# Performance work log

Hardware: AMD Instinct MI355X
Metric: run time of the kernel (lower is better)

Reference implementation:

```python
import jax, jax.numpy as jnp
import numpy as np

EMBED_DIM = 1024
B, S = 4, 2048
SCALE = float(np.sqrt(EMBED_DIM))


def setup_inputs() -> dict:
    key = jax.random.key(0)
    ks = jax.random.split(key, 9)
    d = EMBED_DIM
    init = 1.0 / np.sqrt(d)
    return {
        "query": jax.random.normal(ks[0], (B, S, d), jnp.float32),
        "key": jax.random.normal(ks[1], (B, S, d), jnp.float32),
        "value": jax.random.normal(ks[2], (B, S, d), jnp.float32),
        "wq": jax.random.uniform(ks[3], (d, d), jnp.float32, -init, init),
        "bq": jax.random.uniform(ks[4], (d,), jnp.float32, -init, init),
        "wk": jax.random.uniform(ks[5], (d, d), jnp.float32, -init, init),
        "bk": jax.random.uniform(ks[6], (d,), jnp.float32, -init, init),
        "wv": jax.random.uniform(ks[7], (d, d), jnp.float32, -init, init),
        "bv": jax.random.uniform(ks[8], (d,), jnp.float32, -init, init),
    }


def reference(query, key, value, wq, bq, wk, bk, wv, bv):
    # Linear projections (torch Linear: x @ W^T + b; here weights stored as [in, out])
    q = query @ wq + bq            # [B,S,D]
    k = key @ wk + bk              # [B,S,D]
    v = value @ wv + bv            # [B,S,D]
    scores = jnp.einsum("bqd,bkd->bqk", q, k) / SCALE   # [B,S,S]
    attn = jax.nn.softmax(scores, axis=-1)
    # dropout in eval mode -> identity
    return jnp.einsum("bqk,bkd->bqd", attn, v)          # [B,S,D]
```

## Files before the change

kernel.cpp:

```cpp
#include <hip/hip_runtime.h>
#include <hip/hip_bf16.h>

typedef __attribute__((ext_vector_type(4))) float   f32x4;
typedef __attribute__((ext_vector_type(8))) __bf16  bf16x8;
typedef __attribute__((ext_vector_type(4))) __bf16  bf16x4;

#define NB 4
#define SS 2048
#define DD 1024

__device__ __forceinline__ void gload_lds16(const void* g, void* l) {
  __builtin_amdgcn_global_load_lds((const __attribute__((address_space(1))) void*)g,
                                   (__attribute__((address_space(3))) void*)l,
                                   16, 0, 0);
}

__global__ __launch_bounds__(256) void prep_w_kernel(
    const float* __restrict__ wq, const float* __restrict__ wk, const float* __restrict__ wv,
    const float* __restrict__ bq, const float* __restrict__ bk, const float* __restrict__ bv,
    __bf16* __restrict__ Wt, float* __restrict__ biasbuf)
{
  const int z = blockIdx.z;
  const float* W  = z == 0 ? wq : (z == 1 ? wk : wv);
  const float* bi = z == 0 ? bq : (z == 1 ? bk : bv);
  __bf16* dst = Wt + (size_t)z * (size_t)(DD * DD);
  const int n0 = blockIdx.x * 32, k0 = blockIdx.y * 32;
  __shared__ float t[32][33];
  const int tx = threadIdx.x & 31, ty = threadIdx.x >> 5;
  #pragma unroll
  for (int i = 0; i < 4; i++)
    t[ty + 8 * i][tx] = W[(size_t)(k0 + ty + 8 * i) * DD + n0 + tx];
  __syncthreads();
  #pragma unroll
  for (int i = 0; i < 4; i++)
    dst[(size_t)(n0 + ty + 8 * i) * DD + k0 + tx] = (__bf16)t[tx][ty + 8 * i];
  if (blockIdx.x == 0 && blockIdx.y == 0) {
    #pragma unroll
    for (int i = 0; i < 4; i++)
      biasbuf[z * DD + threadIdx.x + 256 * i] = bi[threadIdx.x + 256 * i];
  }
}


#define PJ_A_OFF(BUF)     ((BUF) * 16384)
#define PJ_B_OFF(BUF, NH) (32768 + ((BUF)*2 + (NH)) * 16384)

#define PJ_DSA(BUF)                                                             \
  _Pragma("unroll") for (int mi = 0; mi < 4; ++mi) {                            \
    _Pragma("unroll") for (int ks = 0; ks < 2; ++ks)                            \
      af[mi][ks] = *(const bf16x8*)(smem + PJ_A_OFF(BUF) + ara[ks] + mi * 2048); }

#define PJ_DSB(DST, BUF, NH)                                                    \
  _Pragma("unroll") for (int ni = 0; ni < 2; ++ni) {                            \
    _Pragma("unroll") for (int ks = 0; ks < 2; ++ks)                            \
      DST[ni][ks] = *(const bf16x8*)(smem + PJ_B_OFF(BUF, NH) + brb2[ks] + ni * 2048); }

#define PJ_GLA(V0, V1, V2, V3, T) do { int t_ = (T); if (t_ >= 16) t_ = 0;      \
  const float* g_ = Ablk + (size_t)t_ * 64;                                     \
  V0 = *(const float4*)(g_ + aoffF0); V1 = *(const float4*)(g_ + aoffF0 + 4);   \
  V2 = *(const float4*)(g_ + aoffF1); V3 = *(const float4*)(g_ + aoffF1 + 4);   \
  __builtin_amdgcn_sched_barrier(0); } while (0)

#define PJ_WRA(BUF, V0, V1, V2, V3) do {                                        \
  bf16x8 w0_, w1_;                                                              \
  w0_[0]=(__bf16)V0.x; w0_[1]=(__bf16)V0.y; w0_[2]=(__bf16)V0.z; w0_[3]=(__bf16)V0.w; \
  w0_[4]=(__bf16)V1.x; w0_[5]=(__bf16)V1.y; w0_[6]=(__bf16)V1.z; w0_[7]=(__bf16)V1.w; \
  w1_[0]=(__bf16)V2.x; w1_[1]=(__bf16)V2.y; w1_[2]=(__bf16)V2.z; w1_[3]=(__bf16)V2.w; \
  w1_[4]=(__bf16)V3.x; w1_[5]=(__bf16)V3.y; w1_[6]=(__bf16)V3.z; w1_[7]=(__bf16)V3.w; \
  *(bf16x8*)(smem + PJ_A_OFF(BUF) + tid * 16) = w0_;                            \
  *(bf16x8*)(smem + PJ_A_OFF(BUF) + 8192 + tid * 16) = w1_; } while (0)

#define PJ_SB0(BUF, T) do { int t_ = (T); if (t_ >= 16) t_ = 0;                 \
  const __bf16* gB_ = Bblk + (size_t)t_ * 64;                                   \
  gload_lds16(gB_ + boff0, smem + PJ_B_OFF(BUF, 0) + tid * 16);                 \
  gload_lds16(gB_ + boff1, smem + PJ_B_OFF(BUF, 0) + 8192 + tid * 16); } while (0)

#define PJ_SB1(BUF, T) do { int t_ = (T); if (t_ >= 16) t_ = 0;                 \
  const __bf16* gB_ = Bblk + (size_t)(128 * 1024) + (size_t)t_ * 64;            \
  gload_lds16(gB_ + boff0, smem + PJ_B_OFF(BUF, 1) + tid * 16);                 \
  gload_lds16(gB_ + boff1, smem + PJ_B_OFF(BUF, 1) + 8192 + tid * 16); } while (0)

#define PJ_MFMA(BF, NH) do {                                                    \
  __builtin_amdgcn_s_barrier();                                                 \
  asm volatile("s_waitcnt lgkmcnt(0)" ::: "memory");                            \
  __builtin_amdgcn_sched_barrier(0);                                            \
  __builtin_amdgcn_s_setprio(1);                                                \
  _Pragma("unroll") for (int mi = 0; mi < 4; ++mi)                              \
  _Pragma("unroll") for (int ni = 0; ni < 2; ++ni)                              \
  _Pragma("unroll") for (int ks = 0; ks < 2; ++ks)                              \
    acc[mi][(NH)*2+ni] = __builtin_amdgcn_mfma_f32_16x16x32_bf16(               \
        af[mi][ks], BF[ni][ks], acc[mi][(NH)*2+ni], 0, 0, 0);                   \
  __builtin_amdgcn_s_setprio(0);                                                \
  __builtin_amdgcn_sched_barrier(0);                                            \
  __builtin_amdgcn_s_barrier(); } while (0)

__global__ __launch_bounds__(512) void proj_kernel(
    const float* __restrict__ Xq, const float* __restrict__ Xk, const float* __restrict__ Xv,
    const __bf16* __restrict__ Wt, const float* __restrict__ bias,
    __bf16* __restrict__ Qo, __bf16* __restrict__ Ko, __bf16* __restrict__ Vt)
{
  extern __shared__ char smem[];

  const int gx = gridDim.x, gy = gridDim.y;
  const int nwg = gx * gy * gridDim.z;
  int lin = blockIdx.x + gx * (blockIdx.y + gy * blockIdx.z);
  const int cpx = nwg >> 3;
  int swz = (lin & 7) * cpx + (lin >> 3);
  const int bx = swz % gx;
  int rem = swz / gx;
  const int by = rem % gy;
  const int bz = rem / gy;

  const long brow = (long)by * 128, bcol = (long)bx * 256;
  const float* Xsel = bz == 0 ? Xq : (bz == 1 ? Xk : Xv);
  const float* Ablk = Xsel + (size_t)brow * 1024;
  const __bf16* Bblk = Wt + (size_t)bz * (DD * DD) + (size_t)bcol * 1024;

  const int tid  = threadIdx.x;
  const int lane = tid & 63;
  const int wid  = tid >> 6;
  const int wm = wid >> 2, wn = wid & 3;
  const int l15 = lane & 15, l4 = lane >> 4;
  const int lx = (lane & 7) << 4;

  int aoffF0, aoffF1;
  #pragma unroll
  for (int i = 0; i < 2; ++i) {
    const int p = i * 8192 + tid * 16;
    const int r = p >> 7;
    const int kb = (p ^ ((r & 7) << 4)) & 127;
    const int aF = r * 1024 + (kb >> 1);
    if (i == 0) aoffF0 = aF; else aoffF1 = aF;
  }
  int boff0, boff1;
  #pragma unroll
  for (int i = 0; i < 2; ++i) {
    const int p = i * 8192 + tid * 16;
    const int r = p >> 7;
    const int kb = (p ^ ((r & 7) << 4)) & 127;
    const int off = r * 1024 + (kb >> 1);
    if (i == 0) boff0 = off; else boff1 = off;
  }

  int ara[2], brb2[2];
  #pragma unroll
  for (int ks = 0; ks < 2; ++ks) {
    ara[ks]  = ((((wm * 64 + l15) * 64 + l4 * 8) * 2) + ks * 64) ^ lx;
    brb2[ks] = ((((wn * 32 + l15) * 64 + l4 * 8) * 2) + ks * 64) ^ lx;
  }

  f32x4 acc[4][4] = {};
  bf16x8 af[4][2], b0[2][2], b1[2][2];
  float4 La0, La1, La2, La3, Lb0, Lb1, Lb2, Lb3;

  PJ_GLA(La0, La1, La2, La3, 0);
  PJ_GLA(Lb0, Lb1, Lb2, Lb3, 1);
  PJ_SB0(0, 0); PJ_SB1(0, 0); PJ_SB0(1, 1);
  asm volatile("s_waitcnt vmcnt(10)" ::: "memory");
  PJ_WRA(0, La0, La1, La2, La3);
  asm volatile("s_waitcnt vmcnt(6)" ::: "memory");
  PJ_WRA(1, Lb0, Lb1, Lb2, Lb3);
  asm volatile("s_waitcnt vmcnt(2) lgkmcnt(0)" ::: "memory");
  __builtin_amdgcn_s_barrier();

  for (int it = 0; it < 8; ++it) {
    const int tt = it * 2;
    PJ_GLA(La0, La1, La2, La3, tt + 2);
    PJ_SB1(1, tt + 1);
    PJ_DSA(0); PJ_DSB(b0, 0, 0);
    PJ_MFMA(b0, 0);
    PJ_SB0(0, tt + 2);
    asm volatile("s_waitcnt vmcnt(10)" ::: "memory");
    PJ_DSB(b1, 0, 1);
    PJ_MFMA(b1, 1);
    asm volatile("s_waitcnt vmcnt(4)" ::: "memory");
    PJ_WRA(0, La0, La1, La2, La3);
    PJ_GLA(Lb0, Lb1, Lb2, Lb3, tt + 3);
    PJ_SB1(0, tt + 2);
    PJ_DSA(1); PJ_DSB(b0, 1, 0);
    PJ_MFMA(b0, 0);
    PJ_SB0(1, tt + 3);
    asm volatile("s_waitcnt vmcnt(4)" ::: "memory");
    PJ_WRA(1, Lb0, Lb1, Lb2, Lb3);
    PJ_DSB(b1, 1, 1);
    PJ_MFMA(b1, 1);
  }

  if (bz == 2) {
    #pragma unroll
    for (int mi = 0; mi < 4; ++mi) {
      #pragma unroll
      for (int n = 0; n < 4; ++n) {
        const long row = brow + wm * 64 + mi * 16 + l4 * 4;
        const long col = bcol + (n >> 1) * 128 + wn * 32 + (n & 1) * 16 + l15;
        const float bvv = bias[2 * DD + col];
        const long bb = row >> 11, s = row & 2047;
        bf16x4 pk = { (__bf16)(acc[mi][n][0] + bvv), (__bf16)(acc[mi][n][1] + bvv),
                      (__bf16)(acc[mi][n][2] + bvv), (__bf16)(acc[mi][n][3] + bvv) };
        *(bf16x4*)&Vt[bb * 2097152 + col * 2048 + s] = pk;
      }
    }
  } else {
    __bf16* C = bz == 0 ? Qo : Ko;
    #pragma unroll
    for (int mi = 0; mi < 4; ++mi) {
      #pragma unroll
      for (int n = 0; n < 4; ++n) {
        const long row = brow + wm * 64 + mi * 16 + l4 * 4;
        const long col = bcol + (n >> 1) * 128 + wn * 32 + (n & 1) * 16 + l15;
        const float bvv = bias[bz * DD + col];
        #pragma unroll
        for (int e = 0; e < 4; ++e)
          C[(row + e) * 1024 + col] = (__bf16)(acc[mi][n][e] + bvv);
      }
    }
  }
}


#define A_OFF(BUF, MH) (((BUF)*2 + (MH)) * 16384)
#define B_OFF(BUF, NH) (65536 + ((BUF)*2 + (NH)) * 16384)

#define STAGE_A(BUF, MH, T) do { int t_ = (T); if (t_ >= NT) t_ = 0;            \
  const __bf16* gs_ = Ablk + (size_t)(MH) * (64 * (size_t)lda) + (size_t)t_ * 64; \
  gload_lds16(gs_ + aoff0, smem + A_OFF(BUF, MH) + tid * 16);                    \
  gload_lds16(gs_ + aoff1, smem + A_OFF(BUF, MH) + 8192 + tid * 16); } while (0)

#define STAGE_B(BUF, NH, T) do { int t_ = (T); if (t_ >= NT) t_ = 0;            \
  const __bf16* gs_ = Bblk + (size_t)(NH) * (32 * (size_t)ldb) + (size_t)t_ * 64; \
  gload_lds16(gs_ + boff0, smem + B_OFF(BUF, NH) + tid * 16);                    \
  gload_lds16(gs_ + boff1, smem + B_OFF(BUF, NH) + 8192 + tid * 16); } while (0)

#define DSREAD_A(DST, BUF, MH)                                                  \
  _Pragma("unroll") for (int mi = 0; mi < 4; ++mi) {                            \
    _Pragma("unroll") for (int ks = 0; ks < 2; ++ks)                            \
      DST[mi][ks] = *(const bf16x8*)(smem + A_OFF(BUF, MH) + arb[ks] + mi * 2048); }

#define DSREAD_BS(DST, BUF, NH)                                                 \
  _Pragma("unroll") for (int ni = 0; ni < 2; ++ni) {                            \
    _Pragma("unroll") for (int ks = 0; ks < 2; ++ks)                            \
      DST[ni][ks] = *(const bf16x8*)(smem + B_OFF(BUF, NH) + brb[ks] + ni * 2048); }

#define BARRIER_MFMA(AF, BF, MH, NH) do {                                       \
  __builtin_amdgcn_s_barrier();                                                 \
  asm volatile("s_waitcnt lgkmcnt(0)" ::: "memory");                            \
  __builtin_amdgcn_sched_barrier(0);                                            \
  __builtin_amdgcn_s_setprio(1);                                                \
  _Pragma("unroll") for (int mi = 0; mi < 4; ++mi)                              \
  _Pragma("unroll") for (int ni = 0; ni < 2; ++ni)                              \
  _Pragma("unroll") for (int ks = 0; ks < 2; ++ks)                              \
    acc[(MH)*4+mi][(NH)*2+ni] = __builtin_amdgcn_mfma_f32_16x16x32_bf16(        \
        AF[mi][ks], BF[ni][ks], acc[(MH)*4+mi][(NH)*2+ni], 0, 0, 0);            \
  __builtin_amdgcn_s_setprio(0);                                                \
  __builtin_amdgcn_sched_barrier(0);                                            \
  __builtin_amdgcn_s_barrier(); } while (0)

__global__ __launch_bounds__(512) void gemm8p_kernel(
    const __bf16* __restrict__ A, const __bf16* __restrict__ B,
    float scale, void* __restrict__ Cout,
    int K, int lda, int ldb, int ldc,
    long strideA, long strideB, long strideC)
{
  extern __shared__ char smem[];

  const int gx = gridDim.x, gy = gridDim.y;
  const int nwg = gx * gy * gridDim.z;
  int lin = blockIdx.x + gx * (blockIdx.y + gy * blockIdx.z);
  const int cpx = nwg >> 3;
  int swz = (lin & 7) * cpx + (lin >> 3);
  const int bx = swz % gx;
  int rem = swz / gx;
  const int by = rem % gy;
  const int bz = rem / gy;

  const long brow = (long)by * 256, bcol = (long)bx * 256;
  const __bf16* Ablk = A + (size_t)bz * strideA + (size_t)brow * lda;
  const __bf16* Bblk = B + (size_t)bz * strideB + (size_t)bcol * ldb;

  const int tid  = threadIdx.x;
  const int lane = tid & 63;
  const int wid  = tid >> 6;
  const int wm = wid >> 2, wn = wid & 3;
  const int l15 = lane & 15, l4 = lane >> 4;
  const int lx = (lane & 7) << 4;

  const int NT = K >> 6;
  const int niter = NT >> 1;

  int aoff0, aoff1, boff0, boff1;
  #pragma unroll
  for (int i = 0; i < 2; ++i) {
    const int p = i * 8192 + tid * 16;
    const int l = p ^ (((p >> 7) & 7) << 4);
    const int r = p >> 7;
    const int kb = l & 127;
    const int av = ((r >> 6) * 128 + (r & 63)) * lda + (kb >> 1);
    const int bv = ((r >> 5) * 64 + (r & 31)) * ldb + (kb >> 1);
    if (i == 0) { aoff0 = av; boff0 = bv; } else { aoff1 = av; boff1 = bv; }
  }

  int arb[2], brb[2];
  #pragma unroll
  for (int ks = 0; ks < 2; ++ks) {
    arb[ks] = ((((wm * 64 + l15) * 64 + l4 * 8) * 2) + ks * 64) ^ lx;
    brb[ks] = ((((wn * 32 + l15) * 64 + l4 * 8) * 2) + ks * 64) ^ lx;
  }

  f32x4 acc[8][4] = {};
  bf16x8 a0[4][2], a1[4][2], b0[2][2], b1[2][2];

  STAGE_B(0, 0, 0); STAGE_A(0, 0, 0); STAGE_A(0, 1, 0); STAGE_B(0, 1, 0);
  STAGE_B(1, 0, 1); STAGE_A(1, 0, 1);
  asm volatile("s_waitcnt vmcnt(4)" ::: "memory");
  __builtin_amdgcn_s_barrier();

  for (int it = 0; it < niter; ++it) {
    const int tt = it * 2;
    DSREAD_A(a0, 0, 0); DSREAD_BS(b0, 0, 0);
    STAGE_A(1, 1, tt + 1);
    BARRIER_MFMA(a0, b0, 0, 0);
    DSREAD_A(a1, 0, 1);
    STAGE_B(1, 1, tt + 1);
    BARRIER_MFMA(a1, b0, 1, 0);
    DSREAD_BS(b1, 0, 1);
    STAGE_B(0, 0, tt + 2);
    BARRIER_MFMA(a0, b1, 0, 1);
    STAGE_A(0, 0, tt + 2);
    asm volatile("s_waitcnt vmcnt(4)" ::: "memory");
    BARRIER_MFMA(a1, b1, 1, 1);
    DSREAD_A(a0, 1, 0); DSREAD_BS(b0, 1, 0);
    STAGE_A(0, 1, tt + 2);
    BARRIER_MFMA(a0, b0, 0, 0);
    DSREAD_A(a1, 1, 1);
    STAGE_B(0, 1, tt + 2);
    BARRIER_MFMA(a1, b0, 1, 0);
    DSREAD_BS(b1, 1, 1);
    STAGE_B(1, 0, tt + 3);
    BARRIER_MFMA(a0, b1, 0, 1);
    STAGE_A(1, 0, tt + 3);
    asm volatile("s_waitcnt vmcnt(4)" ::: "memory");
    BARRIER_MFMA(a1, b1, 1, 1);
  }

  const int cr = l4 * 4;
  __bf16* C = (__bf16*)Cout + (size_t)bz * strideC;
  #pragma unroll
  for (int m = 0; m < 8; ++m) {
    #pragma unroll
    for (int n = 0; n < 4; ++n) {
      const long row = brow + wm * 128 + m * 16 + cr;
      const long col = bcol + wn * 64 + n * 16 + l15;
      #pragma unroll
      for (int e = 0; e < 4; ++e)
        C[(row + e) * (size_t)ldc + col] = (__bf16)__expf(acc[m][n][e] * scale);
    }
  }
}


#define PV_A_OFF(BUF)     ((BUF) * 16384)
#define PV_B_OFF(BUF, NH) (32768 + ((BUF)*2 + (NH)) * 16384)

#define PV_DSA(BUF)                                                             \
  _Pragma("unroll") for (int mi = 0; mi < 4; ++mi) {                            \
    _Pragma("unroll") for (int ks = 0; ks < 2; ++ks)                            \
      af[mi][ks] = *(const bf16x8*)(smem + PV_A_OFF(BUF) + ara[ks] + mi * 2048); }

#define PV_DSB(DST, BUF, NH)                                                    \
  _Pragma("unroll") for (int ni = 0; ni < 2; ++ni) {                            \
    _Pragma("unroll") for (int ks = 0; ks < 2; ++ks)                            \
      DST[ni][ks] = *(const bf16x8*)(smem + PV_B_OFF(BUF, NH) + brb2[ks] + ni * 2048); }

#define PV_SA(BUF, T) do { int t_ = (T); if (t_ >= NT) t_ = 0;                  \
  const __bf16* gA_ = Ablk + (size_t)t_ * 64;                                   \
  gload_lds16(gA_ + aoff0, smem + PV_A_OFF(BUF) + tid * 16);                    \
  gload_lds16(gA_ + aoff1, smem + PV_A_OFF(BUF) + 8192 + tid * 16);             \
  const __bf16* gB_ = Bblk + (size_t)t_ * 64;                                   \
  gload_lds16(gB_ + boff0, smem + PV_B_OFF(BUF, 0) + tid * 16);                 \
  gload_lds16(gB_ + boff1, smem + PV_B_OFF(BUF, 0) + 8192 + tid * 16); } while (0)

#define PV_SB(BUF, T) do { int t_ = (T); if (t_ >= NT) t_ = 0;                  \
  const __bf16* gB_ = Bblk + (size_t)(128 * (size_t)ldb) + (size_t)t_ * 64;     \
  gload_lds16(gB_ + boff0, smem + PV_B_OFF(BUF, 1) + tid * 16);                 \
  gload_lds16(gB_ + boff1, smem + PV_B_OFF(BUF, 1) + 8192 + tid * 16); } while (0)

#define PV_MFMA(BF, NH, DOSUM) do {                                             \
  __builtin_amdgcn_s_barrier();                                                 \
  asm volatile("s_waitcnt lgkmcnt(0)" ::: "memory");                            \
  __builtin_amdgcn_sched_barrier(0);                                            \
  __builtin_amdgcn_s_setprio(1);                                                \
  _Pragma("unroll") for (int mi = 0; mi < 4; ++mi)                              \
  _Pragma("unroll") for (int ni = 0; ni < 2; ++ni)                              \
  _Pragma("unroll") for (int ks = 0; ks < 2; ++ks)                              \
    acc[mi][(NH)*2+ni] = __builtin_amdgcn_mfma_f32_16x16x32_bf16(               \
        af[mi][ks], BF[ni][ks], acc[mi][(NH)*2+ni], 0, 0, 0);                   \
  if (DOSUM) {                                                                  \
    _Pragma("unroll") for (int mi = 0; mi < 4; ++mi)                            \
    _Pragma("unroll") for (int ks = 0; ks < 2; ++ks)                            \
      accs[mi] = __builtin_amdgcn_mfma_f32_16x16x32_bf16(                       \
          af[mi][ks], onesf, accs[mi], 0, 0, 0); }                              \
  __builtin_amdgcn_s_setprio(0);                                                \
  __builtin_amdgcn_sched_barrier(0);                                            \
  __builtin_amdgcn_s_barrier(); } while (0)

__global__ __launch_bounds__(512) void gemm128_kernel(
    const __bf16* __restrict__ A, const __bf16* __restrict__ B,
    void* __restrict__ Cout,
    int K, int lda, int ldb, int ldc,
    long strideA, long strideB, long strideC)
{
  extern __shared__ char smem[];

  const int gx = gridDim.x, gy = gridDim.y;
  const int nwg = gx * gy * gridDim.z;
  int lin = blockIdx.x + gx * (blockIdx.y + gy * blockIdx.z);
  const int cpx = nwg >> 3;
  int swz = (lin & 7) * cpx + (lin >> 3);
  const int bx = swz % gx;
  int rem = swz / gx;
  const int by = rem % gy;
  const int bz = rem / gy;

  const long brow = (long)by * 128, bcol = (long)bx * 256;
  const __bf16* Ablk = A + (size_t)bz * strideA + (size_t)brow * lda;
  const __bf16* Bblk = B + (size_t)bz * strideB + (size_t)bcol * ldb;

  const int tid  = threadIdx.x;
  const int lane = tid & 63;
  const int wid  = tid >> 6;
  const int wm = wid >> 2, wn = wid & 3;
  const int l15 = lane & 15, l4 = lane >> 4;
  const int lx = (lane & 7) << 4;

  const int NT = K >> 6;
  const int niter = NT >> 1;

  int aoff0, aoff1, boff0, boff1;
  #pragma unroll
  for (int i = 0; i < 2; ++i) {
    const int p = i * 8192 + tid * 16;
    const int r = p >> 7;
    const int kb = (p ^ ((r & 7) << 4)) & 127;
    const int av = r * lda + (kb >> 1);
    const int bv = r * ldb + (kb >> 1);
    if (i == 0) { aoff0 = av; boff0 = bv; } else { aoff1 = av; boff1 = bv; }
  }

  int ara[2], brb2[2];
  #pragma unroll
  for (int ks = 0; ks < 2; ++ks) {
    ara[ks]  = ((((wm * 64 + l15) * 64 + l4 * 8) * 2) + ks * 64) ^ lx;
    brb2[ks] = ((((wn * 32 + l15) * 64 + l4 * 8) * 2) + ks * 64) ^ lx;
  }

  f32x4 acc[4][4] = {};
  f32x4 accs[4] = {};
  bf16x8 af[4][2], b0[2][2], b1[2][2];
  bf16x8 onesf;
  #pragma unroll
  for (int j = 0; j < 8; ++j) onesf[j] = (__bf16)1.0f;

  PV_SA(0, 0); PV_SB(0, 0); PV_SA(1, 1);
  asm volatile("s_waitcnt vmcnt(6)" ::: "memory");
  __builtin_amdgcn_s_barrier();

  for (int it = 0; it < niter; ++it) {
    const int tt = it * 2;
    PV_SB(1, tt + 1);
    asm volatile("s_waitcnt vmcnt(6)" ::: "memory");
    PV_DSA(0); PV_DSB(b0, 0, 0);
    PV_MFMA(b0, 0, 1);
    PV_SA(0, tt + 2);
    asm volatile("s_waitcnt vmcnt(6)" ::: "memory");
    PV_DSB(b1, 0, 1);
    PV_MFMA(b1, 1, 0);
    PV_SB(0, tt + 2);
    asm volatile("s_waitcnt vmcnt(6)" ::: "memory");
    PV_DSA(1); PV_DSB(b0, 1, 0);
    PV_MFMA(b0, 0, 1);
    PV_SA(1, tt + 3);
    asm volatile("s_waitcnt vmcnt(6)" ::: "memory");
    PV_DSB(b1, 1, 1);
    PV_MFMA(b1, 1, 0);
  }

  float* C = (float*)Cout + (size_t)bz * strideC;
  #pragma unroll
  for (int mi = 0; mi < 4; ++mi) {
    f32x4 inv;
    #pragma unroll
    for (int e = 0; e < 4; ++e) inv[e] = 1.0f / accs[mi][e];
    #pragma unroll
    for (int n = 0; n < 4; ++n) {
      const long row = brow + wm * 64 + mi * 16 + l4 * 4;
      const long col = bcol + (n >> 1) * 128 + wn * 32 + (n & 1) * 16 + l15;
      #pragma unroll
      for (int e = 0; e < 4; ++e)
        C[(row + e) * (size_t)ldc + col] = acc[mi][n][e] * inv[e];
    }
  }
}

extern "C" void kernel_launch(void* const* d_in, const int* in_sizes, int n_in,
                              void* d_out, int out_size, void* d_ws, size_t ws_size,
                              hipStream_t stream)
{
  const float* query = (const float*)d_in[0];
  const float* key   = (const float*)d_in[1];
  const float* value = (const float*)d_in[2];
  const float* wq = (const float*)d_in[3];
  const float* bq = (const float*)d_in[4];
  const float* wk = (const float*)d_in[5];
  const float* bk = (const float*)d_in[6];
  const float* wv = (const float*)d_in[7];
  const float* bv = (const float*)d_in[8];

  char* ws = (char*)d_ws;
  __bf16* P       = (__bf16*)(ws + 0);
  __bf16* Wt      = (__bf16*)(ws + 33554432);
  float*  biasbuf = (float*)(ws + 39845888);
  __bf16* Qb      = (__bf16*)(ws + 39858176);
  __bf16* Kb      = (__bf16*)(ws + 56635392);
  __bf16* Vt      = (__bf16*)(ws + 73412608);

  hipFuncSetAttribute((const void*)proj_kernel,    hipFuncAttributeMaxDynamicSharedMemorySize, 131072);
  hipFuncSetAttribute((const void*)gemm8p_kernel,  hipFuncAttributeMaxDynamicSharedMemorySize, 131072);
  hipFuncSetAttribute((const void*)gemm128_kernel, hipFuncAttributeMaxDynamicSharedMemorySize, 131072);

  dim3 b256(256), b512(512);

  prep_w_kernel<<<dim3(32, 32, 3), b256, 0, stream>>>(wq, wk, wv, bq, bk, bv, Wt, biasbuf);

  proj_kernel<<<dim3(4, 64, 3), b512, 98304, stream>>>(
      query, key, value, Wt, biasbuf, Qb, Kb, Vt);

  gemm8p_kernel<<<dim3(8, 8, 4), b512, 131072, stream>>>(
      Qb, Kb, 0.03125f, P,
      1024, 1024, 1024, 2048,
      2097152L, 2097152L, 4194304L);

  gemm128_kernel<<<dim3(4, 16, 4), b512, 98304, stream>>>(
      P, Vt, d_out,
      2048, 2048, 2048, 1024,
      4194304L, 2097152L, 2097152L);

  (void)in_sizes; (void)n_in; (void)out_size; (void)ws_size;
}
```

Measured before the change: 169.1 us.

## Pre-convert fp32 activations to bf16 and stream projection A tiles via direct LDS loads

Adds a separate kernel that converts query, key and value from fp32 to bf16 into workspace. The projection GEMM then loads both A and B tiles with global-to-LDS async loads, dropping the register staging and in-loop fp32-to-bf16 conversion along with its VGPR pressure. The cost is an extra pass over 100MB of fp32 input plus writing 50MB of bf16, which may outweigh the simpler pipeline since the projection re-reads each A tile only a few times.

```diff
diff --git a/kernel.cpp b/kernel.cpp
--- a/kernel.cpp
+++ b/kernel.cpp
@@ -13,6 +13,18 @@
   __builtin_amdgcn_global_load_lds((const __attribute__((address_space(1))) void*)g,
                                    (__attribute__((address_space(3))) void*)l,
                                    16, 0, 0);
+}
+
+__global__ __launch_bounds__(256) void cvt_in_kernel(
+    const float* __restrict__ q, const float* __restrict__ k,
+    const float* __restrict__ v, __bf16* __restrict__ X)
+{
+  const float* src = blockIdx.z == 0 ? q : (blockIdx.z == 1 ? k : v);
+  __bf16* dst = X + (size_t)blockIdx.z * (size_t)(NB * SS * DD);
+  size_t i = ((size_t)blockIdx.x * 256 + threadIdx.x) * 4;
+  float4 f = *(const float4*)&src[i];
+  bf16x4 o = { (__bf16)f.x, (__bf16)f.y, (__bf16)f.z, (__bf16)f.w };
+  *(bf16x4*)&dst[i] = o;
 }
 
 __global__ __launch_bounds__(256) void prep_w_kernel(
@@ -55,27 +67,15 @@
     _Pragma("unroll") for (int ks = 0; ks < 2; ++ks)                            \
       DST[ni][ks] = *(const bf16x8*)(smem + PJ_B_OFF(BUF, NH) + brb2[ks] + ni * 2048); }
 
-#define PJ_GLA(V0, V1, V2, V3, T) do { int t_ = (T); if (t_ >= 16) t_ = 0;      \
-  const float* g_ = Ablk + (size_t)t_ * 64;                                     \
-  V0 = *(const float4*)(g_ + aoffF0); V1 = *(const float4*)(g_ + aoffF0 + 4);   \
-  V2 = *(const float4*)(g_ + aoffF1); V3 = *(const float4*)(g_ + aoffF1 + 4);   \
-  __builtin_amdgcn_sched_barrier(0); } while (0)
-
-#define PJ_WRA(BUF, V0, V1, V2, V3) do {                                        \
-  bf16x8 w0_, w1_;                                                              \
-  w0_[0]=(__bf16)V0.x; w0_[1]=(__bf16)V0.y; w0_[2]=(__bf16)V0.z; w0_[3]=(__bf16)V0.w; \
-  w0_[4]=(__bf16)V1.x; w0_[5]=(__bf16)V1.y; w0_[6]=(__bf16)V1.z; w0_[7]=(__bf16)V1.w; \
-  w1_[0]=(__bf16)V2.x; w1_[1]=(__bf16)V2.y; w1_[2]=(__bf16)V2.z; w1_[3]=(__bf16)V2.w; \
-  w1_[4]=(__bf16)V3.x; w1_[5]=(__bf16)V3.y; w1_[6]=(__bf16)V3.z; w1_[7]=(__bf16)V3.w; \
-  *(bf16x8*)(smem + PJ_A_OFF(BUF) + tid * 16) = w0_;                            \
-  *(bf16x8*)(smem + PJ_A_OFF(BUF) + 8192 + tid * 16) = w1_; } while (0)
-
-#define PJ_SB0(BUF, T) do { int t_ = (T); if (t_ >= 16) t_ = 0;                 \
+#define PJ_SA(BUF, T) do { int t_ = (T); if (t_ >= 16) t_ = 0;                  \
+  const __bf16* gA_ = Ablk + (size_t)t_ * 64;                                   \
+  gload_lds16(gA_ + aoff0, smem + PJ_A_OFF(BUF) + tid * 16);                    \
+  gload_lds16(gA_ + aoff1, smem + PJ_A_OFF(BUF) + 8192 + tid * 16);             \
   const __bf16* gB_ = Bblk + (size_t)t_ * 64;                                   \
   gload_lds16(gB_ + boff0, smem + PJ_B_OFF(BUF, 0) + tid * 16);                 \
   gload_lds16(gB_ + boff1, smem + PJ_B_OFF(BUF, 0) + 8192 + tid * 16); } while (0)
 
-#define PJ_SB1(BUF, T) do { int t_ = (T); if (t_ >= 16) t_ = 0;                 \
+#define PJ_SB(BUF, T) do { int t_ = (T); if (t_ >= 16) t_ = 0;                  \
   const __bf16* gB_ = Bblk + (size_t)(128 * 1024) + (size_t)t_ * 64;            \
   gload_lds16(gB_ + boff0, smem + PJ_B_OFF(BUF, 1) + tid * 16);                 \
   gload_lds16(gB_ + boff1, smem + PJ_B_OFF(BUF, 1) + 8192 + tid * 16); } while (0)
@@ -95,8 +95,8 @@
   __builtin_amdgcn_s_barrier(); } while (0)
 
 __global__ __launch_bounds__(512) void proj_kernel(
-    const float* __restrict__ Xq, const float* __restrict__ Xk, const float* __restrict__ Xv,
-    const __bf16* __restrict__ Wt, const float* __restrict__ bias,
+    const __bf16* __restrict__ X, const __bf16* __restrict__ Wt,
+    const float* __restrict__ bias,
     __bf16* __restrict__ Qo, __bf16* __restrict__ Ko, __bf16* __restrict__ Vt)
 {
   extern __shared__ char smem[];
@@ -112,9 +112,8 @@
   const int bz = rem / gy;
 
   const long brow = (long)by * 128, bcol = (long)bx * 256;
-  const float* Xsel = bz == 0 ? Xq : (bz == 1 ? Xk : Xv);
-  const float* Ablk = Xsel + (size_t)brow * 1024;
-  const __bf16* Bblk = Wt + (size_t)bz * (DD * DD) + (size_t)bcol * 1024;
+  const __bf16* Ablk = X + (size_t)bz * 8388608 + (size_t)brow * 1024;
+  const __bf16* Bblk = Wt + (size_t)bz * 1048576 + (size_t)bcol * 1024;
 
   const int tid  = threadIdx.x;
   const int lane = tid & 63;
@@ -123,23 +122,14 @@
   const int l15 = lane & 15, l4 = lane >> 4;
   const int lx = (lane & 7) << 4;
 
-  int aoffF0, aoffF1;
-  #pragma unroll
-  for (int i = 0; i < 2; ++i) {
-    const int p = i * 8192 + tid * 16;
-    const int r = p >> 7;
-    const int kb = (p ^ ((r & 7) << 4)) & 127;
-    const int aF = r * 1024 + (kb >> 1);
-    if (i == 0) aoffF0 = aF; else aoffF1 = aF;
-  }
-  int boff0, boff1;
+  int aoff0, aoff1, boff0, boff1;
   #pragma unroll
   for (int i = 0; i < 2; ++i) {
     const int p = i * 8192 + tid * 16;
     const int r = p >> 7;
     const int kb = (p ^ ((r & 7) << 4)) & 127;
     const int off = r * 1024 + (kb >> 1);
-    if (i == 0) boff0 = off; else boff1 = off;
+    if (i == 0) { aoff0 = off; boff0 = off; } else { aoff1 = off; boff1 = off; }
   }
 
   int ara[2], brb2[2];
@@ -151,37 +141,27 @@
 
   f32x4 acc[4][4] = {};
   bf16x8 af[4][2], b0[2][2], b1[2][2];
-  float4 La0, La1, La2, La3, Lb0, Lb1, Lb2, Lb3;
-
-  PJ_GLA(La0, La1, La2, La3, 0);
-  PJ_GLA(Lb0, Lb1, Lb2, Lb3, 1);
-  PJ_SB0(0, 0); PJ_SB1(0, 0); PJ_SB0(1, 1);
-  asm volatile("s_waitcnt vmcnt(10)" ::: "memory");
-  PJ_WRA(0, La0, La1, La2, La3);
+
+  PJ_SA(0, 0); PJ_SB(0, 0); PJ_SA(1, 1);
   asm volatile("s_waitcnt vmcnt(6)" ::: "memory");
-  PJ_WRA(1, Lb0, Lb1, Lb2, Lb3);
-  asm volatile("s_waitcnt vmcnt(2) lgkmcnt(0)" ::: "memory");
   __builtin_amdgcn_s_barrier();
 
   for (int it = 0; it < 8; ++it) {
     const int tt = it * 2;
-    PJ_GLA(La0, La1, La2, La3, tt + 2);
-    PJ_SB1(1, tt + 1);
+    PJ_SB(1, tt + 1);
+    asm volatile("s_waitcnt vmcnt(6)" ::: "memory");
     PJ_DSA(0); PJ_DSB(b0, 0, 0);
     PJ_MFMA(b0, 0);
-    PJ_SB0(0, tt + 2);
-    asm volatile("s_waitcnt vmcnt(10)" ::: "memory");
+    PJ_SA(0, tt + 2);
+    asm volatile("s_waitcnt vmcnt(6)" ::: "memory");
     PJ_DSB(b1, 0, 1);
     PJ_MFMA(b1, 1);
-    asm volatile("s_waitcnt vmcnt(4)" ::: "memory");
-    PJ_WRA(0, La0, La1, La2, La3);
-    PJ_GLA(Lb0, Lb1, Lb2, Lb3, tt + 3);
-    PJ_SB1(0, tt + 2);
+    PJ_SB(0, tt + 2);
+    asm volatile("s_waitcnt vmcnt(6)" ::: "memory");
     PJ_DSA(1); PJ_DSB(b0, 1, 0);
     PJ_MFMA(b0, 0);
-    PJ_SB0(1, tt + 3);
-    asm volatile("s_waitcnt vmcnt(4)" ::: "memory");
-    PJ_WRA(1, Lb0, Lb1, Lb2, Lb3);
+    PJ_SA(1, tt + 3);
+    asm volatile("s_waitcnt vmcnt(6)" ::: "memory");
     PJ_DSB(b1, 1, 1);
     PJ_MFMA(b1, 1);
   }
@@ -516,12 +496,13 @@
   const float* bv = (const float*)d_in[8];
 
   char* ws = (char*)d_ws;
-  __bf16* P       = (__bf16*)(ws + 0);
-  __bf16* Wt      = (__bf16*)(ws + 33554432);
-  float*  biasbuf = (float*)(ws + 39845888);
-  __bf16* Qb      = (__bf16*)(ws + 39858176);
-  __bf16* Kb      = (__bf16*)(ws + 56635392);
-  __bf16* Vt      = (__bf16*)(ws + 73412608);
+  __bf16* Xbf     = (__bf16*)(ws + 0);
+  __bf16* Wt      = (__bf16*)(ws + 50331648);
+  float*  biasbuf = (float*)(ws + 56623104);
+  __bf16* Qb      = (__bf16*)(ws + 56635392);
+  __bf16* Kb      = (__bf16*)(ws + 73412608);
+  __bf16* Vt      = (__bf16*)(ws + 90189824);
+  __bf16* P       = Xbf;
 
   hipFuncSetAttribute((const void*)proj_kernel,    hipFuncAttributeMaxDynamicSharedMemorySize, 131072);
   hipFuncSetAttribute((const void*)gemm8p_kernel,  hipFuncAttributeMaxDynamicSharedMemorySize, 131072);
@@ -529,16 +510,14 @@
 
   dim3 b256(256), b512(512);
 
+  cvt_in_kernel<<<dim3(8192, 1, 3), b256, 0, stream>>>(query, key, value, Xbf);
   prep_w_kernel<<<dim3(32, 32, 3), b256, 0, stream>>>(wq, wk, wv, bq, bk, bv, Wt, biasbuf);
-
   proj_kernel<<<dim3(4, 64, 3), b512, 98304, stream>>>(
-      query, key, value, Wt, biasbuf, Qb, Kb, Vt);
-
+      Xbf, Wt, biasbuf, Qb, Kb, Vt);
   gemm8p_kernel<<<dim3(8, 8, 4), b512, 131072, stream>>>(
       Qb, Kb, 0.03125f, P,
       1024, 1024, 1024, 2048,
       2097152L, 2097152L, 4194304L);
-
   gemm128_kernel<<<dim3(4, 16, 4), b512, 98304, stream>>>(
       P, Vt, d_out,
       2048, 2048, 2048, 1024,
```

After: 173.1 us. +2.4%, slower.
